# Kernel tuning notes

Measured on AMD Instinct MI355X. Metric: run time of the kernel, lower is better.

Reference implementation:

```python
import jax, jax.numpy as jnp
import numpy as np

N_NODES = 50000
N_EDGES = 262144
HID = 256
N_CLS = 2


def setup_inputs() -> dict:
    key = jax.random.key(0)
    ks = jax.random.split(key, 6)
    node_repr = jax.random.normal(ks[0], (N_NODES, HID), dtype=jnp.float32)
    src = jax.random.randint(ks[1], (N_EDGES,), 0, N_NODES, dtype=jnp.int64)
    dst = jax.random.randint(ks[2], (N_EDGES,), 0, N_NODES, dtype=jnp.int64)
    # Linear weights stored as (in, out); init ~ torch default scale
    W1 = jax.random.normal(ks[3], (4 * HID, 2 * HID), dtype=jnp.float32) * (1.0 / np.sqrt(4 * HID))
    b1 = jnp.zeros((2 * HID,), dtype=jnp.float32)
    W2 = jax.random.normal(ks[4], (2 * HID, N_CLS), dtype=jnp.float32) * (1.0 / np.sqrt(2 * HID))
    b2 = jnp.zeros((N_CLS,), dtype=jnp.float32)
    return {"node_repr": node_repr, "src": src, "dst": dst,
            "W1": W1, "b1": b1, "W2": W2, "b2": b2}


def reference(node_repr, src, dst, W1, b1, W2, b2):
    h_i = node_repr[src]                      # [E, H] gather
    h_j = node_repr[dst]                      # [E, H] gather
    edge_input = jnp.concatenate(
        [h_i, h_j, jnp.abs(h_i - h_j), h_i * h_j], axis=1)  # [E, 4H]
    h = jax.nn.relu(edge_input @ W1 + b1)     # [E, 2H]; dropout = identity (eval)
    return h @ W2 + b2                        # [E, C]
```

## Files before the change

kernel.cpp:

```cpp
#include <hip/hip_runtime.h>

#define N_NODES 50000
#define E_EDGES 262144

typedef __attribute__((ext_vector_type(8))) _Float16 f16x8;
typedef __attribute__((ext_vector_type(2))) _Float16 f16x2;
typedef __attribute__((ext_vector_type(4))) float f32x4;

union V16 { uint4 u; f16x8 h; };
union U32 { unsigned u; f16x2 p; };

__device__ __forceinline__ unsigned h2pack(float a, float b) {
  union { _Float16 h[2]; unsigned u; } r;
  r.h[0] = (_Float16)a;
  r.h[1] = (_Float16)b;
  return r.u;
}
__device__ __forceinline__ void async_gather16(const void* gptr, void* lptr) {
  __builtin_amdgcn_global_load_lds(
      (const __attribute__((address_space(1))) void*)gptr,
      (__attribute__((address_space(3))) void*)lptr, 16, 0, 0);
}

__global__ void cvt_node_kernel(const float* __restrict__ x, unsigned short* __restrict__ y) {
  int i = (blockIdx.x * 256 + threadIdx.x) * 8;
  float4 f0 = *(const float4*)(x + i);
  float4 f1 = *(const float4*)(x + i + 4);
  uint4 o;
  o.x = h2pack(f0.x, f0.y);
  o.y = h2pack(f0.z, f0.w);
  o.z = h2pack(f1.x, f1.y);
  o.w = h2pack(f1.z, f1.w);
  *(uint4*)(y + i) = o;
}

__global__ void prep_w1pp2_kernel(const float* __restrict__ w1, unsigned short* __restrict__ w1pp2) {
  int t = blockIdx.x * 256 + threadIdx.x;
  int step = t >> 13;
  int rem = t & 8191;
  int sq = rem >> 9;
  int col = rem & 511;
  int s = sq >> 2, qd = sq & 3;
  int k0 = s * 256 + step * 32 + qd * 8;
  float f[8];
#pragma unroll
  for (int i = 0; i < 8; ++i) f[i] = w1[(size_t)(k0 + i) * 512 + col];
  uint4 o;
  o.x = h2pack(f[0], f[1]);
  o.y = h2pack(f[2], f[3]);
  o.z = h2pack(f[4], f[5]);
  o.w = h2pack(f[6], f[7]);
  *(uint4*)(w1pp2 + (size_t)t * 8) = o;
}

__global__ void init_out_kernel(float* __restrict__ out, const float* __restrict__ b2) {
  int i = blockIdx.x * 256 + threadIdx.x;
  float2 v; v.x = b2[0]; v.y = b2[1];
  *(float2*)(out + (size_t)i * 2) = v;
}

__global__ __launch_bounds__(512, 2) void edge_mlp_kernel(
    const unsigned short* __restrict__ nodeb,
    const unsigned short* __restrict__ w1pp2,
    const int* __restrict__ src,
    const int* __restrict__ dst,
    const float* __restrict__ b1,
    const float* __restrict__ w2,
    float* __restrict__ out) {
  __shared__ char smem[65536];

  const int tid = threadIdx.x;
  const int wid = tid >> 6;
  const int lane = tid & 63;
  const int quad = lane >> 4;
  const int l16 = lane & 15;
  const int bx = blockIdx.x;
  const int xc = bx & 7;
  const int m_idx = (bx >> 3) * 8 + xc;
  const int row0 = m_idx * 64;
  const int n0 = wid * 64;

  const char* nodeB = (const char*)nodeb;
  const char* w1B = (const char*)w1pp2;

  const unsigned bQ = (unsigned)(quad * 8192 + (n0 + l16) * 16);
  const char* w1s = w1B;

  const unsigned aXor = (unsigned)(l16 & 7);
  const unsigned aBase = (unsigned)(l16 * 512);

  f32x4 acc[4][4];
#pragma unroll
  for (int mt = 0; mt < 4; ++mt)
#pragma unroll
    for (int nt = 0; nt < 4; ++nt)
      acc[mt][nt] = (f32x4){0.f, 0.f, 0.f, 0.f};

  {
    const int eh = tid >> 5;
    const unsigned wsw = (unsigned)(((tid & 31) ^ (eh & 7)) << 4);
#pragma unroll
    for (int c = 0; c < 4; ++c) {
      int e = c * 16 + eh;
      unsigned so = ((unsigned)src[row0 + e] << 9) + wsw;
      unsigned do_ = ((unsigned)dst[row0 + e] << 9) + wsw;
      async_gather16(nodeB + so, smem + c * 8192 + wid * 1024);
      async_gather16(nodeB + do_, smem + 32768 + c * 8192 + wid * 1024);
    }
  }
  __syncthreads();

#pragma unroll 2
  for (int step = 0; step < 8; ++step) {
    V16 bf[4][4];
#pragma unroll
    for (int s = 0; s < 4; ++s)
#pragma unroll
      for (int nt = 0; nt < 4; ++nt)
        bf[s][nt].u = *(const uint4*)(w1s + (bQ + (unsigned)(s * 32768 + nt * 256)));
    const unsigned stq = (unsigned)(step * 4 + quad);
    V16 hi[4], hj[4];
#pragma unroll
    for (int mt = 0; mt < 4; ++mt) {
      unsigned ao = (unsigned)(mt * 16 * 512) + aBase + ((stq ^ aXor) << 4);
      hi[mt].u = *(const uint4*)(smem + ao);
      hj[mt].u = *(const uint4*)(smem + 32768 + ao);
    }
#pragma unroll
    for (int mt = 0; mt < 4; ++mt)
#pragma unroll
      for (int nt = 0; nt < 4; ++nt)
        acc[mt][nt] = __builtin_amdgcn_mfma_f32_16x16x32_f16(hi[mt].h, bf[0][nt].h, acc[mt][nt], 0, 0, 0);
#pragma unroll
    for (int mt = 0; mt < 4; ++mt)
#pragma unroll
      for (int nt = 0; nt < 4; ++nt)
        acc[mt][nt] = __builtin_amdgcn_mfma_f32_16x16x32_f16(hj[mt].h, bf[1][nt].h, acc[mt][nt], 0, 0, 0);
#pragma unroll
    for (int mt = 0; mt < 4; ++mt) {
      const unsigned hw[4] = {hi[mt].u.x, hi[mt].u.y, hi[mt].u.z, hi[mt].u.w};
      const unsigned jw[4] = {hj[mt].u.x, hj[mt].u.y, hj[mt].u.z, hj[mt].u.w};
      unsigned d[4], pr[4];
#pragma unroll
      for (int w = 0; w < 4; ++w) {
        U32 hx, jx, dd, pp;
        hx.u = hw[w];
        jx.u = jw[w];
        dd.p = hx.p - jx.p;
        d[w] = dd.u & 0x7fff7fffu;
        pp.p = hx.p * jx.p;
        pr[w] = pp.u;
      }
      V16 a2, a3;
      a2.u = make_uint4(d[0], d[1], d[2], d[3]);
      a3.u = make_uint4(pr[0], pr[1], pr[2], pr[3]);
#pragma unroll
      for (int nt = 0; nt < 4; ++nt)
        acc[mt][nt] = __builtin_amdgcn_mfma_f32_16x16x32_f16(a2.h, bf[2][nt].h, acc[mt][nt], 0, 0, 0);
#pragma unroll
      for (int nt = 0; nt < 4; ++nt)
        acc[mt][nt] = __builtin_amdgcn_mfma_f32_16x16x32_f16(a3.h, bf[3][nt].h, acc[mt][nt], 0, 0, 0);
    }
    w1s += 131072;
  }

#pragma unroll
  for (int mt = 0; mt < 4; ++mt) {
    float pc0[4] = {0.f, 0.f, 0.f, 0.f};
    float pc1[4] = {0.f, 0.f, 0.f, 0.f};
#pragma unroll
    for (int nt = 0; nt < 4; ++nt) {
      int gc = n0 + nt * 16 + l16;
      float b1v = b1[gc];
      float w20 = w2[gc * 2 + 0];
      float w21 = w2[gc * 2 + 1];
#pragma unroll
      for (int r = 0; r < 4; ++r) {
        float v = fmaxf(acc[mt][nt][r] + b1v, 0.f);
        pc0[r] = fmaf(v, w20, pc0[r]);
        pc1[r] = fmaf(v, w21, pc1[r]);
      }
    }
#pragma unroll
    for (int r = 0; r < 4; ++r) {
      float s0 = pc0[r], s1 = pc1[r];
#pragma unroll
      for (int off = 1; off < 16; off <<= 1) {
        s0 += __shfl_xor(s0, off);
        s1 += __shfl_xor(s1, off);
      }
      int e = row0 + mt * 16 + quad * 4 + r;
      if (l16 == 0) unsafeAtomicAdd(&out[(size_t)e * 2 + 0], s0);
      if (l16 == 1) unsafeAtomicAdd(&out[(size_t)e * 2 + 1], s1);
    }
  }
}

extern "C" void kernel_launch(void* const* d_in, const int* in_sizes, int n_in,
                              void* d_out, int out_size, void* d_ws, size_t ws_size,
                              hipStream_t stream) {
  const float* node = (const float*)d_in[0];
  const int* src = (const int*)d_in[1];
  const int* dst = (const int*)d_in[2];
  const float* W1 = (const float*)d_in[3];
  const float* b1 = (const float*)d_in[4];
  const float* W2 = (const float*)d_in[5];
  const float* b2 = (const float*)d_in[6];
  float* out = (float*)d_out;

  unsigned short* nodeb = (unsigned short*)d_ws;
  unsigned short* w1pp2 = (unsigned short*)((char*)d_ws + 25600000);

  cvt_node_kernel<<<6250, 256, 0, stream>>>(node, nodeb);
  prep_w1pp2_kernel<<<256, 256, 0, stream>>>(W1, w1pp2);
  init_out_kernel<<<1024, 256, 0, stream>>>(out, b2);
  edge_mlp_kernel<<<4096, 512, 0, stream>>>(nodeb, w1pp2, src, dst, b1, W2, out);
}
```

Before: 417.8 us.

## Precompute per-node W1 projections for h_i and h_j and gather per edge

Splits the first linear layer so the h_i and h_j blocks of W1 are applied once per node in a new kernel, storing two fp16 projection tables. The edge kernel then only does the |h_i-h_j| and h_i*h_j MFMAs and adds gathered per-node projections in the epilogue. This halves edge-side matrix work in exchange for an extra node GEMM, large table writes, scattered 2-byte gathers, and extra fp16 rounding of partial sums. The occupancy hint on the edge kernel is also relaxed.

```diff
diff --git a/kernel.cpp b/kernel.cpp
--- a/kernel.cpp
+++ b/kernel.cpp
@@ -2,6 +2,7 @@
 
 #define N_NODES 50000
 #define E_EDGES 262144
+#define P_ROWS 50048
 
 typedef __attribute__((ext_vector_type(8))) _Float16 f16x8;
 typedef __attribute__((ext_vector_type(2))) _Float16 f16x2;
@@ -59,9 +60,91 @@
   *(float2*)(out + (size_t)i * 2) = v;
 }
 
-__global__ __launch_bounds__(512, 2) void edge_mlp_kernel(
+__global__ __launch_bounds__(256) void node_pab_kernel(
     const unsigned short* __restrict__ nodeb,
     const unsigned short* __restrict__ w1pp2,
+    unsigned short* __restrict__ Pab) {
+  __shared__ char smem[32768];
+  const int tid = threadIdx.x;
+  const int wid = tid >> 6;
+  const int lane = tid & 63;
+  const int quad = lane >> 4;
+  const int l16 = lane & 15;
+  const int bx = blockIdx.x;
+  const int table = bx & 1;
+  const int half = (bx >> 1) & 1;
+  const int ntile = bx >> 2;
+  const int nrow0 = ntile * 64;
+  const int cb = half * 256 + wid * 64;
+
+  const char* nodeB = (const char*)nodeb;
+  const char* w1B = (const char*)w1pp2;
+
+  const unsigned bQ = (unsigned)((table * 4 + quad) * 8192 + (cb + l16) * 16);
+  const unsigned aXor = (unsigned)(l16 & 7);
+  const unsigned aBase = (unsigned)(l16 * 512);
+
+  f32x4 acc[4][4];
+#pragma unroll
+  for (int mt = 0; mt < 4; ++mt)
+#pragma unroll
+    for (int nt = 0; nt < 4; ++nt)
+      acc[mt][nt] = (f32x4){0.f, 0.f, 0.f, 0.f};
+
+  {
+    const int eh = tid >> 5;
+    const unsigned wsw = (unsigned)(((tid & 31) ^ (eh & 7)) << 4);
+#pragma unroll
+    for (int c = 0; c < 8; ++c) {
+      int e = c * 8 + eh;
+      int n = nrow0 + e;
+      if (n > N_NODES - 1) n = N_NODES - 1;
+      unsigned so = ((unsigned)n << 9) + wsw;
+      async_gather16(nodeB + so, smem + c * 4096 + wid * 1024);
+    }
+  }
+  __syncthreads();
+
+  const char* w1s = w1B;
+#pragma unroll 2
+  for (int step = 0; step < 8; ++step) {
+    V16 bf[4];
+#pragma unroll
+    for (int nt = 0; nt < 4; ++nt)
+      bf[nt].u = *(const uint4*)(w1s + (bQ + (unsigned)(nt * 256)));
+    const unsigned stq = (unsigned)(step * 4 + quad);
+    V16 hi[4];
+#pragma unroll
+    for (int mt = 0; mt < 4; ++mt) {
+      unsigned ao = (unsigned)(mt * 16 * 512) + aBase + ((stq ^ aXor) << 4);
+      hi[mt].u = *(const uint4*)(smem + ao);
+    }
+#pragma unroll
+    for (int mt = 0; mt < 4; ++mt)
+#pragma unroll
+      for (int nt = 0; nt < 4; ++nt)
+        acc[mt][nt] = __builtin_amdgcn_mfma_f32_16x16x32_f16(hi[mt].h, bf[nt].h, acc[mt][nt], 0, 0, 0);
+    w1s += 131072;
+  }
+
+  unsigned short* Pt = Pab + (size_t)table * ((size_t)P_ROWS * 512);
+#pragma unroll
+  for (int mt = 0; mt < 4; ++mt)
+#pragma unroll
+    for (int nt = 0; nt < 4; ++nt)
+#pragma unroll
+      for (int r = 0; r < 4; ++r) {
+        int prow = nrow0 + mt * 16 + quad * 4 + r;
+        int pc = cb + nt * 16 + l16;
+        _Float16 v = (_Float16)acc[mt][nt][r];
+        Pt[(size_t)prow * 512 + pc] = *(unsigned short*)&v;
+      }
+}
+
+__global__ __launch_bounds__(512) void edge_mlp_kernel(
+    const unsigned short* __restrict__ nodeb,
+    const unsigned short* __restrict__ w1pp2,
+    const unsigned short* __restrict__ Pab,
     const int* __restrict__ src,
     const int* __restrict__ dst,
     const float* __restrict__ b1,
@@ -112,12 +195,12 @@
 
 #pragma unroll 2
   for (int step = 0; step < 8; ++step) {
-    V16 bf[4][4];
-#pragma unroll
-    for (int s = 0; s < 4; ++s)
+    V16 bf2[2][4];
+#pragma unroll
+    for (int s2 = 0; s2 < 2; ++s2)
 #pragma unroll
       for (int nt = 0; nt < 4; ++nt)
-        bf[s][nt].u = *(const uint4*)(w1s + (bQ + (unsigned)(s * 32768 + nt * 256)));
+        bf2[s2][nt].u = *(const uint4*)(w1s + (bQ + (unsigned)((s2 + 2) * 32768 + nt * 256)));
     const unsigned stq = (unsigned)(step * 4 + quad);
     V16 hi[4], hj[4];
 #pragma unroll
@@ -126,16 +209,6 @@
       hi[mt].u = *(const uint4*)(smem + ao);
       hj[mt].u = *(const uint4*)(smem + 32768 + ao);
     }
-#pragma unroll
-    for (int mt = 0; mt < 4; ++mt)
-#pragma unroll
-      for (int nt = 0; nt < 4; ++nt)
-        acc[mt][nt] = __builtin_amdgcn_mfma_f32_16x16x32_f16(hi[mt].h, bf[0][nt].h, acc[mt][nt], 0, 0, 0);
-#pragma unroll
-    for (int mt = 0; mt < 4; ++mt)
-#pragma unroll
-      for (int nt = 0; nt < 4; ++nt)
-        acc[mt][nt] = __builtin_amdgcn_mfma_f32_16x16x32_f16(hj[mt].h, bf[1][nt].h, acc[mt][nt], 0, 0, 0);
 #pragma unroll
     for (int mt = 0; mt < 4; ++mt) {
       const unsigned hw[4] = {hi[mt].u.x, hi[mt].u.y, hi[mt].u.z, hi[mt].u.w};
@@ -156,16 +229,25 @@
       a3.u = make_uint4(pr[0], pr[1], pr[2], pr[3]);
 #pragma unroll
       for (int nt = 0; nt < 4; ++nt)
-        acc[mt][nt] = __builtin_amdgcn_mfma_f32_16x16x32_f16(a2.h, bf[2][nt].h, acc[mt][nt], 0, 0, 0);
+        acc[mt][nt] = __builtin_amdgcn_mfma_f32_16x16x32_f16(a2.h, bf2[0][nt].h, acc[mt][nt], 0, 0, 0);
 #pragma unroll
       for (int nt = 0; nt < 4; ++nt)
-        acc[mt][nt] = __builtin_amdgcn_mfma_f32_16x16x32_f16(a3.h, bf[3][nt].h, acc[mt][nt], 0, 0, 0);
+        acc[mt][nt] = __builtin_amdgcn_mfma_f32_16x16x32_f16(a3.h, bf2[1][nt].h, acc[mt][nt], 0, 0, 0);
     }
     w1s += 131072;
   }
 
+  const unsigned short* Pa = Pab;
+  const unsigned short* Pb = Pab + (size_t)P_ROWS * 512;
 #pragma unroll
   for (int mt = 0; mt < 4; ++mt) {
+    int si[4], di[4];
+#pragma unroll
+    for (int r = 0; r < 4; ++r) {
+      int e = row0 + mt * 16 + quad * 4 + r;
+      si[r] = src[e];
+      di[r] = dst[e];
+    }
     float pc0[4] = {0.f, 0.f, 0.f, 0.f};
     float pc1[4] = {0.f, 0.f, 0.f, 0.f};
 #pragma unroll
@@ -176,7 +258,9 @@
       float w21 = w2[gc * 2 + 1];
 #pragma unroll
       for (int r = 0; r < 4; ++r) {
-        float v = fmaxf(acc[mt][nt][r] + b1v, 0.f);
+        float pa = (float)*(const _Float16*)(Pa + (size_t)si[r] * 512 + gc);
+        float pb = (float)*(const _Float16*)(Pb + (size_t)di[r] * 512 + gc);
+        float v = fmaxf(acc[mt][nt][r] + pa + pb + b1v, 0.f);
         pc0[r] = fmaf(v, w20, pc0[r]);
         pc1[r] = fmaf(v, w21, pc1[r]);
       }
@@ -210,9 +294,11 @@
 
   unsigned short* nodeb = (unsigned short*)d_ws;
   unsigned short* w1pp2 = (unsigned short*)((char*)d_ws + 25600000);
+  unsigned short* Pab   = (unsigned short*)((char*)d_ws + 26648576);
 
   cvt_node_kernel<<<6250, 256, 0, stream>>>(node, nodeb);
   prep_w1pp2_kernel<<<256, 256, 0, stream>>>(W1, w1pp2);
+  node_pab_kernel<<<3128, 256, 0, stream>>>(nodeb, w1pp2, Pab);
   init_out_kernel<<<1024, 256, 0, stream>>>(out, b2);
-  edge_mlp_kernel<<<4096, 512, 0, stream>>>(nodeb, w1pp2, src, dst, b1, W2, out);
-}
+  edge_mlp_kernel<<<4096, 512, 0, stream>>>(nodeb, w1pp2, Pab, src, dst, b1, W2, out);
+}
```

After: 441.6 us. 1.06x slower.

## Merge prep kernels and replace output atomics with LDS cross-wave reduction

Applied to the files above, without the earlier changes.

Folds the node and W1 conversion kernels into one launch and drops the output-init kernel. The edge kernel now reduces the per-wave second-layer partial sums through shared memory, adds b2, and writes each output row once instead of issuing global atomics. This removes two launches and the atomic traffic on the output, at the cost of two extra block barriers and relaxed launch bounds (the minimum of two blocks per CU is removed).

```diff
diff --git a/kernel.cpp b/kernel.cpp
--- a/kernel.cpp
+++ b/kernel.cpp
@@ -22,50 +22,48 @@
       (__attribute__((address_space(3))) void*)lptr, 16, 0, 0);
 }
 
-__global__ void cvt_node_kernel(const float* __restrict__ x, unsigned short* __restrict__ y) {
-  int i = (blockIdx.x * 256 + threadIdx.x) * 8;
-  float4 f0 = *(const float4*)(x + i);
-  float4 f1 = *(const float4*)(x + i + 4);
-  uint4 o;
-  o.x = h2pack(f0.x, f0.y);
-  o.y = h2pack(f0.z, f0.w);
-  o.z = h2pack(f1.x, f1.y);
-  o.w = h2pack(f1.z, f1.w);
-  *(uint4*)(y + i) = o;
-}
-
-__global__ void prep_w1pp2_kernel(const float* __restrict__ w1, unsigned short* __restrict__ w1pp2) {
-  int t = blockIdx.x * 256 + threadIdx.x;
-  int step = t >> 13;
-  int rem = t & 8191;
-  int sq = rem >> 9;
-  int col = rem & 511;
-  int s = sq >> 2, qd = sq & 3;
-  int k0 = s * 256 + step * 32 + qd * 8;
-  float f[8];
-#pragma unroll
-  for (int i = 0; i < 8; ++i) f[i] = w1[(size_t)(k0 + i) * 512 + col];
-  uint4 o;
-  o.x = h2pack(f[0], f[1]);
-  o.y = h2pack(f[2], f[3]);
-  o.z = h2pack(f[4], f[5]);
-  o.w = h2pack(f[6], f[7]);
-  *(uint4*)(w1pp2 + (size_t)t * 8) = o;
-}
-
-__global__ void init_out_kernel(float* __restrict__ out, const float* __restrict__ b2) {
-  int i = blockIdx.x * 256 + threadIdx.x;
-  float2 v; v.x = b2[0]; v.y = b2[1];
-  *(float2*)(out + (size_t)i * 2) = v;
-}
-
-__global__ __launch_bounds__(512, 2) void edge_mlp_kernel(
+__global__ __launch_bounds__(256) void prep_all_kernel(
+    const float* __restrict__ node, const float* __restrict__ w1,
+    unsigned short* __restrict__ nodeb, unsigned short* __restrict__ w1pp2) {
+  const int bx = blockIdx.x;
+  if (bx < 6250) {
+    int i = (bx * 256 + threadIdx.x) * 8;
+    float4 f0 = *(const float4*)(node + i);
+    float4 f1 = *(const float4*)(node + i + 4);
+    uint4 o;
+    o.x = h2pack(f0.x, f0.y);
+    o.y = h2pack(f0.z, f0.w);
+    o.z = h2pack(f1.x, f1.y);
+    o.w = h2pack(f1.z, f1.w);
+    *(uint4*)(nodeb + i) = o;
+  } else {
+    int t = (bx - 6250) * 256 + threadIdx.x;
+    int step = t >> 13;
+    int rem = t & 8191;
+    int sq = rem >> 9;
+    int col = rem & 511;
+    int s = sq >> 2, qd = sq & 3;
+    int k0 = s * 256 + step * 32 + qd * 8;
+    float f[8];
+#pragma unroll
+    for (int i = 0; i < 8; ++i) f[i] = w1[(size_t)(k0 + i) * 512 + col];
+    uint4 o;
+    o.x = h2pack(f[0], f[1]);
+    o.y = h2pack(f[2], f[3]);
+    o.z = h2pack(f[4], f[5]);
+    o.w = h2pack(f[6], f[7]);
+    *(uint4*)(w1pp2 + (size_t)t * 8) = o;
+  }
+}
+
+__global__ __launch_bounds__(512) void edge_mlp_kernel(
     const unsigned short* __restrict__ nodeb,
     const unsigned short* __restrict__ w1pp2,
     const int* __restrict__ src,
     const int* __restrict__ dst,
     const float* __restrict__ b1,
     const float* __restrict__ w2,
+    const float* __restrict__ b2,
     float* __restrict__ out) {
   __shared__ char smem[65536];
 
@@ -164,6 +162,8 @@
     w1s += 131072;
   }
 
+  float* red = (float*)smem;
+  __syncthreads();
 #pragma unroll
   for (int mt = 0; mt < 4; ++mt) {
     float pc0[4] = {0.f, 0.f, 0.f, 0.f};
@@ -189,10 +189,17 @@
         s0 += __shfl_xor(s0, off);
         s1 += __shfl_xor(s1, off);
       }
-      int e = row0 + mt * 16 + quad * 4 + r;
-      if (l16 == 0) unsafeAtomicAdd(&out[(size_t)e * 2 + 0], s0);
-      if (l16 == 1) unsafeAtomicAdd(&out[(size_t)e * 2 + 1], s1);
-    }
+      int el = mt * 16 + quad * 4 + r;
+      if (l16 == 0) red[wid * 128 + el * 2 + 0] = s0;
+      if (l16 == 1) red[wid * 128 + el * 2 + 1] = s1;
+    }
+  }
+  __syncthreads();
+  if (tid < 128) {
+    float s = b2[tid & 1];
+#pragma unroll
+    for (int w = 0; w < 8; ++w) s += red[w * 128 + tid];
+    out[(size_t)row0 * 2 + tid] = s;
   }
 }
 
@@ -211,8 +218,6 @@
   unsigned short* nodeb = (unsigned short*)d_ws;
   unsigned short* w1pp2 = (unsigned short*)((char*)d_ws + 25600000);
 
-  cvt_node_kernel<<<6250, 256, 0, stream>>>(node, nodeb);
-  prep_w1pp2_kernel<<<256, 256, 0, stream>>>(W1, w1pp2);
-  init_out_kernel<<<1024, 256, 0, stream>>>(out, b2);
-  edge_mlp_kernel<<<4096, 512, 0, stream>>>(nodeb, w1pp2, src, dst, b1, W2, out);
-}
+  prep_all_kernel<<<6506, 256, 0, stream>>>(node, W1, nodeb, w1pp2);
+  edge_mlp_kernel<<<4096, 512, 0, stream>>>(nodeb, w1pp2, src, dst, b1, W2, b2, out);
+}
```

Result: no change. 411.2 us (-1.6%).
